# Kernel optimization log

Measured on AMD Instinct MI355X. Metric: run time of the kernel, lower is better.

Reference implementation:

```python
import jax, jax.numpy as jnp
import numpy as np

D_MODEL = 2048
NUM_HEADS = 16
HEAD_DIM = 128


def setup_inputs() -> dict:
    key = jax.random.key(0)
    ks = jax.random.split(key, 9)
    B, S = 2, 2048
    s_in = 1.0 / np.sqrt(D_MODEL)
    return {
        "x": jax.random.normal(ks[0], (B, S, D_MODEL), dtype=jnp.float32),
        "wq": jax.random.normal(ks[1], (D_MODEL, D_MODEL), dtype=jnp.float32) * s_in,
        "bq": jnp.zeros((D_MODEL,), jnp.float32),
        "wk": jax.random.normal(ks[2], (D_MODEL, HEAD_DIM), dtype=jnp.float32) * s_in,
        "bk": jnp.zeros((HEAD_DIM,), jnp.float32),
        "wv": jax.random.normal(ks[3], (D_MODEL, HEAD_DIM), dtype=jnp.float32) * s_in,
        "bv": jnpp_zeros(ks) if False else jnp.zeros((HEAD_DIM,), jnp.float32),
        "wo": jax.random.normal(ks[4], (D_MODEL, D_MODEL), dtype=jnp.float32) * s_in,
        "bo": jnp.zeros((D_MODEL,), jnp.float32),
    }


def reference(x, wq, bq, wk, bk, wv, bv, wo, bo):
    B, S, _ = x.shape
    H, Dh = NUM_HEADS, HEAD_DIM
    q = (x @ wq + bq).reshape(B, S, H, Dh)          # [B,S,H,Dh]
    k = x @ wk + bk                                  # [B,S,Dh] (single KV head)
    v = x @ wv + bv                                  # [B,S,Dh]
    scale = 1.0 / jnp.sqrt(jnp.asarray(Dh, x.dtype))
    # scores: [B,H,Sq,Sk] — MQA: K shared across heads
    scores = jnp.einsum('bqhd,bkd->bhqk', q, k) * scale
    attn = jax.nn.softmax(scores, axis=-1)
    out = jnp.einsum('bhqk,bkd->bqhd', attn, v).reshape(B, S, H * Dh)
    return out @ wo + bo
```

## Files before the change

kernel.cpp:

```cpp
#include <hip/hip_runtime.h>
#include <stdint.h>

typedef unsigned short u16;

#define D_MODEL 2048
#define HEADS 16
#define HDIM 128
#define SEQ 2048
#define BATCH 2
#define NROWS (BATCH*SEQ)
#define QKV_N (D_MODEL + 2*HDIM)

typedef __attribute__((ext_vector_type(8))) short bf16x8;
typedef __attribute__((ext_vector_type(4))) float f32x4;

__device__ inline u16 f2bf(float f) {
  union { float f; uint32_t u; } v; v.f = f;
  uint32_t r = v.u + 0x7FFFu + ((v.u >> 16) & 1u);
  return (u16)(r >> 16);
}
__device__ inline u16 f2bf_fast(float f) {
  union { float f; uint32_t u; } v; v.f = f;
  return (u16)((v.u + 0x8000u) >> 16);
}

__device__ inline void gload_lds16(const void* g, void* l) {
  __builtin_amdgcn_global_load_lds(
      (const __attribute__((address_space(1))) unsigned int*)g,
      (__attribute__((address_space(3))) unsigned int*)l, 16, 0, 0);
}

__global__ void prep_all(const float* __restrict__ x, u16* __restrict__ xb,
                         const float* __restrict__ wq, const float* __restrict__ wk,
                         const float* __restrict__ wv, const float* __restrict__ wo,
                         u16* __restrict__ wqkvT, u16* __restrict__ woT,
                         const float* __restrict__ bq, const float* __restrict__ bk,
                         const float* __restrict__ bv, float* __restrict__ biasq) {
  const int bid = blockIdx.x, tid = threadIdx.x;
  if (bid < 1024) {
    const float4* xf = (const float4*)x;
    ushort4* xo = (ushort4*)xb;
    int i = bid * 256 + tid;
#pragma unroll
    for (int r = 0; r < 8; r++, i += 262144) {
      float4 f = xf[i];
      ushort4 u;
      u.x = f2bf(f.x); u.y = f2bf(f.y); u.z = f2bf(f.z); u.w = f2bf(f.w);
      xo[i] = u;
    }
  } else if (bid < 9728) {
    __shared__ float t[32][33];
    const int b2 = bid - 1024;
    const int n0v = (b2 % 136) * 32, k0 = (b2 / 136) * 32;
    const float* src; int N, n0, drow; u16* dst;
    if (n0v < 2048)      { src = wq; N = 2048; n0 = n0v;        dst = wqkvT; drow = n0v; }
    else if (n0v < 2176) { src = wk; N = 128;  n0 = n0v - 2048; dst = wqkvT; drow = n0v; }
    else if (n0v < 2304) { src = wv; N = 128;  n0 = n0v - 2176; dst = wqkvT; drow = n0v; }
    else                 { src = wo; N = 2048; n0 = n0v - 2304; dst = woT;   drow = n0v - 2304; }
    const int tx = tid & 31, ty = tid >> 5;
#pragma unroll
    for (int i = 0; i < 4; i++)
      t[ty + 8*i][tx] = src[(size_t)(k0 + ty + 8*i) * N + n0 + tx];
    __syncthreads();
#pragma unroll
    for (int i = 0; i < 4; i++)
      dst[(size_t)(drow + ty + 8*i) * D_MODEL + k0 + tx] = f2bf(t[tx][ty + 8*i]);
  } else {
    for (int i = tid; i < QKV_N; i += 256)
      biasq[i] = (i < D_MODEL) ? bq[i]
               : ((i < D_MODEL + HDIM) ? bk[i - D_MODEL] : bv[i - D_MODEL - HDIM]);
  }
}

#define BM 128
#define BN 128
#define BKK 64

template <bool DB>
__global__ __launch_bounds__(256) void gemm_bt(
    const u16* __restrict__ A, const u16* __restrict__ BT,
    const float* __restrict__ bias,
    u16* __restrict__ Cb, float* __restrict__ Cf,
    u16* __restrict__ vT,
    int M, int N, int tilesN, int K) {
  __shared__ __align__(16) u16 sA[DB ? 2 : 1][BM * BKK];
  __shared__ __align__(16) u16 sB[DB ? 2 : 1][BN * BKK];
  const int tid = threadIdx.x;
  const int wave = tid >> 6, lane = tid & 63;
  const int bm = blockIdx.x / tilesN, bn = blockIdx.x % tilesN;
  const int m0 = bm * BM, n0 = bn * BN;
  const int wm = (wave & 1) * 64, wn = (wave >> 1) * 64;
  const int l16 = lane & 15, quad = lane >> 4;

  f32x4 acc[4][4] = {};

  const int dRow = lane >> 3;
  const int dCol = ((lane & 7) ^ (lane >> 3)) * 8;

#define GDMA(i, buf)                                                           \
  {                                                                            \
    const int _k0 = (i) * BKK;                                                 \
    _Pragma("unroll") for (int c = 0; c < 4; c++) {                            \
      const int op = wave * 4 + c;                                             \
      const int row = op * 8 + dRow;                                           \
      gload_lds16(&A[(size_t)(m0 + row) * K + _k0 + dCol], &sA[buf][op * 512]);\
      gload_lds16(&BT[(size_t)(n0 + row) * K + _k0 + dCol], &sB[buf][op * 512]);\
    }                                                                          \
  }

  const int NI = K / BKK;
  GDMA(0, 0);
  for (int i = 0; i < NI; i++) {
    const int cur = DB ? (i & 1) : 0;
    __syncthreads();
    if (DB && i + 1 < NI) GDMA(i + 1, cur ^ 1);
#pragma unroll
    for (int kk2 = 0; kk2 < 2; kk2++) {
      bf16x8 af[4], bfr[4];
#pragma unroll
      for (int mb = 0; mb < 4; ++mb) {
        const int R = wm + mb * 16 + l16;
        const int s = (kk2 * 4 + quad) ^ (l16 & 7);
        af[mb] = *(const bf16x8*)&sA[cur][R * BKK + s * 8];
      }
#pragma unroll
      for (int nb = 0; nb < 4; ++nb) {
        const int R = wn + nb * 16 + l16;
        const int s = (kk2 * 4 + quad) ^ (l16 & 7);
        bfr[nb] = *(const bf16x8*)&sB[cur][R * BKK + s * 8];
      }
#pragma unroll
      for (int mb = 0; mb < 4; ++mb)
#pragma unroll
        for (int nb = 0; nb < 4; ++nb)
          acc[mb][nb] = __builtin_amdgcn_mfma_f32_16x16x32_bf16(af[mb], bfr[nb], acc[mb][nb], 0, 0, 0);
    }
    if (!DB) {
      __syncthreads();
      if (i + 1 < NI) GDMA(i + 1, 0);
    }
  }
#undef GDMA

#pragma unroll
  for (int mb = 0; mb < 4; ++mb) {
#pragma unroll
    for (int nb = 0; nb < 4; ++nb) {
      const int gn = n0 + wn + nb * 16 + l16;
      const float bb = bias ? bias[gn] : 0.0f;
#pragma unroll
      for (int r = 0; r < 4; ++r) {
        const int gm = m0 + wm + mb * 16 + quad * 4 + r;
        const float v = acc[mb][nb][r] + bb;
        if (Cf) {
          Cf[(size_t)gm * N + gn] = v;
        } else {
          const u16 u = f2bf(v);
          Cb[(size_t)gm * N + gn] = u;
          if (vT && gn >= D_MODEL + HDIM) {
            const int bi = gm >> 11, si = gm & 2047;
            vT[((size_t)bi * HDIM + (gn - D_MODEL - HDIM)) * SEQ + si] = u;
          }
        }
      }
    }
  }
}

__global__ __launch_bounds__(256) void mqa_attn(
    const u16* __restrict__ qkv, const u16* __restrict__ vT, u16* __restrict__ ctx) {
  __shared__ __align__(16) u16 sK[2][64 * 128];
  __shared__ __align__(16) u16 sV[128 * 64];
  __shared__ __align__(16) u16 sP[4][32 * 64];
  const int tid = threadIdx.x, wave = tid >> 6, lane = tid & 63;
  const int qt = blockIdx.x & 15;
  const int h  = (blockIdx.x >> 4) & 15;
  const int b  = blockIdx.x >> 8;
  const int bS = b * SEQ;
  const int q0 = qt * 128 + wave * 32;
  const int l16 = lane & 15, quad = lane >> 4;
  const int sw = l16 & 7;
  u16* myP = &sP[wave][0];

  bf16x8 qf[2][4];
#pragma unroll
  for (int mb = 0; mb < 2; mb++)
#pragma unroll
    for (int kc = 0; kc < 4; kc++)
      qf[mb][kc] = *(const bf16x8*)&qkv[(size_t)(bS + q0 + mb*16 + l16) * QKV_N
                                        + h*HDIM + kc*32 + quad*8];

  f32x4 o[2][8] = {};
  float lrow[2] = {0.f, 0.f};
  const float sc2 = 0.08838834764831845f * 1.4426950408889634f;

  const u16* Kbase = qkv + (size_t)bS * QKV_N + D_MODEL;
  const u16* Vbase = vT + (size_t)b * HDIM * SEQ;

  const int kRowIn = lane >> 4;
  const int kChS   = lane & 15;
  const int vRowIn = lane >> 3;
  const int vChL   = (lane & 7) ^ (lane >> 3);

#define DMA_K(t, dst)                                                          \
  {                                                                            \
    const int _sk = (t) * 64;                                                  \
    _Pragma("unroll") for (int j = 0; j < 4; j++) {                            \
      const int i = wave * 4 + j;                                              \
      const int krow = i * 4 + kRowIn;                                         \
      const int kcl = kChS ^ (krow & 15);                                      \
      gload_lds16(&Kbase[(size_t)(_sk + krow) * QKV_N + kcl * 8],              \
                  &(dst)[i * 512]);                                            \
    }                                                                          \
  }
#define DMA_V(t)                                                               \
  {                                                                            \
    const int _sk = (t) * 64;                                                  \
    _Pragma("unroll") for (int j = 0; j < 4; j++) {                            \
      const int i = wave * 4 + j;                                              \
      const int d = i * 8 + vRowIn;                                            \
      gload_lds16(&Vbase[(size_t)d * SEQ + _sk + vChL * 8], &sV[i * 512]);     \
    }                                                                          \
  }

  DMA_K(0, sK[0]);
  DMA_V(0);
  __syncthreads();

  const int T = SEQ / 64;
  for (int t = 0; t < T; ++t) {
    const int cur = t & 1;
    if (t + 1 < T) DMA_K(t + 1, sK[cur ^ 1]);

    f32x4 sc[2][4];
    __builtin_amdgcn_s_setprio(1);
#pragma unroll
    for (int nb = 0; nb < 4; nb++) {
      bf16x8 kf[4];
#pragma unroll
      for (int kc = 0; kc < 4; kc++)
        kf[kc] = *(const bf16x8*)&sK[cur][(nb*16 + l16) * 128 + (((kc*4 + quad) ^ l16) * 8)];
#pragma unroll
      for (int mb = 0; mb < 2; mb++) {
        f32x4 a = {0.f, 0.f, 0.f, 0.f};
#pragma unroll
        for (int kc = 0; kc < 4; kc++)
          a = __builtin_amdgcn_mfma_f32_16x16x32_bf16(kf[kc], qf[mb][kc], a, 0, 0, 0);
        sc[mb][nb] = a;
      }
    }
    __builtin_amdgcn_s_setprio(0);

#pragma unroll
    for (int mb = 0; mb < 2; mb++)
#pragma unroll
      for (int nb = 0; nb < 4; nb++) {
        float p0 = __builtin_amdgcn_exp2f(sc[mb][nb][0] * sc2);
        float p1 = __builtin_amdgcn_exp2f(sc[mb][nb][1] * sc2);
        float p2 = __builtin_amdgcn_exp2f(sc[mb][nb][2] * sc2);
        float p3 = __builtin_amdgcn_exp2f(sc[mb][nb][3] * sc2);
        lrow[mb] += (p0 + p1) + (p2 + p3);
        uint32_t lo = (uint32_t)f2bf_fast(p0) | ((uint32_t)f2bf_fast(p1) << 16);
        uint32_t hi = (uint32_t)f2bf_fast(p2) | ((uint32_t)f2bf_fast(p3) << 16);
        uint2 w; w.x = lo; w.y = hi;
        const int pr = (nb*2 + (quad >> 1)) ^ sw;
        *(uint2*)&myP[(mb*16 + l16) * 64 + pr * 8 + (quad & 1) * 4] = w;
      }

    __syncthreads();

    bf16x8 pf[2][2];
#pragma unroll
    for (int mb = 0; mb < 2; mb++)
#pragma unroll
      for (int kc = 0; kc < 2; kc++)
        pf[mb][kc] = *(const bf16x8*)&myP[(mb*16 + l16) * 64 + (((kc*4 + quad) ^ sw) * 8)];

    __builtin_amdgcn_s_setprio(1);
#pragma unroll
    for (int nb = 0; nb < 8; nb++) {
      bf16x8 vf[2];
#pragma unroll
      for (int kc = 0; kc < 2; kc++)
        vf[kc] = *(const bf16x8*)&sV[(nb*16 + l16) * 64 + (((kc*4 + quad) ^ (l16 & 7)) * 8)];
#pragma unroll
      for (int mb = 0; mb < 2; mb++)
#pragma unroll
        for (int kc = 0; kc < 2; kc++)
          o[mb][nb] = __builtin_amdgcn_mfma_f32_16x16x32_bf16(pf[mb][kc], vf[kc], o[mb][nb], 0, 0, 0);
    }
    __builtin_amdgcn_s_setprio(0);

    __syncthreads();
    if (t + 1 < T) DMA_V(t + 1);
  }

#pragma unroll
  for (int mb = 0; mb < 2; mb++) {
    lrow[mb] += __shfl_xor(lrow[mb], 16, 64);
    lrow[mb] += __shfl_xor(lrow[mb], 32, 64);
  }
  float invl[2][4];
#pragma unroll
  for (int mb = 0; mb < 2; mb++)
#pragma unroll
    for (int r = 0; r < 4; r++)
      invl[mb][r] = 1.0f / __shfl(lrow[mb], quad * 4 + r, 64);

#pragma unroll
  for (int mb = 0; mb < 2; mb++)
#pragma unroll
    for (int nb = 0; nb < 8; nb++)
#pragma unroll
      for (int r = 0; r < 4; r++) {
        const int gq = q0 + mb*16 + quad*4 + r;
        const int gd = h * HDIM + nb*16 + l16;
        ctx[(size_t)(bS + gq) * D_MODEL + gd] = f2bf(o[mb][nb][r] * invl[mb][r]);
      }
}

extern "C" void kernel_launch(void* const* d_in, const int* in_sizes, int n_in,
                              void* d_out, int out_size, void* d_ws, size_t ws_size,
                              hipStream_t stream) {
  const float* x  = (const float*)d_in[0];
  const float* wq = (const float*)d_in[1];
  const float* bq = (const float*)d_in[2];
  const float* wk = (const float*)d_in[3];
  const float* bk = (const float*)d_in[4];
  const float* wv = (const float*)d_in[5];
  const float* bv = (const float*)d_in[6];
  const float* wo = (const float*)d_in[7];
  const float* bo = (const float*)d_in[8];
  float* out = (float*)d_out;
  char* ws = (char*)d_ws;

  u16*   xb    = (u16*)(ws + 0);
  u16*   wqkvT = (u16*)(ws + 16777216);
  u16*   woT   = (u16*)(ws + 26214400);
  u16*   qkv   = (u16*)(ws + 34603008);
  u16*   vT    = (u16*)(ws + 53477376);
  u16*   ctx   = (u16*)(ws + 54525952);
  float* biasq = (float*)(ws + 71303168);

  prep_all<<<9729, 256, 0, stream>>>(x, xb, wq, wk, wv, wo, wqkvT, woT,
                                     bq, bk, bv, biasq);
  gemm_bt<false><<<32 * 18, 256, 0, stream>>>(xb, wqkvT, biasq, qkv, nullptr, vT,
                                              NROWS, QKV_N, 18, D_MODEL);
  mqa_attn<<<BATCH * HEADS * (SEQ / 128), 256, 0, stream>>>(qkv, vT, ctx);
  gemm_bt<true><<<32 * 16, 256, 0, stream>>>(ctx, woT, bo, nullptr, out, nullptr,
                                             NROWS, D_MODEL, 16, D_MODEL);
}
```

Baseline: 302.1 us.

## Halve attention query tile, read V directly from global, raise occupancy

Result: slower. 464.0 us (+53.6%).

```diff
diff --git a/kernel.cpp b/kernel.cpp
--- a/kernel.cpp
+++ b/kernel.cpp
@@ -167,31 +167,28 @@
   }
 }
 
-__global__ __launch_bounds__(256) void mqa_attn(
+__global__ __launch_bounds__(256, 4) void mqa_attn(
     const u16* __restrict__ qkv, const u16* __restrict__ vT, u16* __restrict__ ctx) {
   __shared__ __align__(16) u16 sK[2][64 * 128];
-  __shared__ __align__(16) u16 sV[128 * 64];
-  __shared__ __align__(16) u16 sP[4][32 * 64];
+  __shared__ __align__(16) u16 sP[4][16 * 64];
   const int tid = threadIdx.x, wave = tid >> 6, lane = tid & 63;
-  const int qt = blockIdx.x & 15;
-  const int h  = (blockIdx.x >> 4) & 15;
-  const int b  = blockIdx.x >> 8;
+  const int qt = blockIdx.x & 31;
+  const int h  = (blockIdx.x >> 5) & 15;
+  const int b  = blockIdx.x >> 9;
   const int bS = b * SEQ;
-  const int q0 = qt * 128 + wave * 32;
+  const int q0 = qt * 64 + wave * 16;
   const int l16 = lane & 15, quad = lane >> 4;
   const int sw = l16 & 7;
   u16* myP = &sP[wave][0];
 
-  bf16x8 qf[2][4];
-#pragma unroll
-  for (int mb = 0; mb < 2; mb++)
-#pragma unroll
-    for (int kc = 0; kc < 4; kc++)
-      qf[mb][kc] = *(const bf16x8*)&qkv[(size_t)(bS + q0 + mb*16 + l16) * QKV_N
-                                        + h*HDIM + kc*32 + quad*8];
-
-  f32x4 o[2][8] = {};
-  float lrow[2] = {0.f, 0.f};
+  bf16x8 qf[4];
+#pragma unroll
+  for (int kc = 0; kc < 4; kc++)
+    qf[kc] = *(const bf16x8*)&qkv[(size_t)(bS + q0 + l16) * QKV_N
+                                  + h*HDIM + kc*32 + quad*8];
+
+  f32x4 o[8] = {};
+  float lrow = 0.f;
   const float sc2 = 0.08838834764831845f * 1.4426950408889634f;
 
   const u16* Kbase = qkv + (size_t)bS * QKV_N + D_MODEL;
@@ -199,8 +196,6 @@
 
   const int kRowIn = lane >> 4;
   const int kChS   = lane & 15;
-  const int vRowIn = lane >> 3;
-  const int vChL   = (lane & 7) ^ (lane >> 3);
 
 #define DMA_K(t, dst)                                                          \
   {                                                                            \
@@ -213,18 +208,8 @@
                   &(dst)[i * 512]);                                            \
     }                                                                          \
   }
-#define DMA_V(t)                                                               \
-  {                                                                            \
-    const int _sk = (t) * 64;                                                  \
-    _Pragma("unroll") for (int j = 0; j < 4; j++) {                            \
-      const int i = wave * 4 + j;                                              \
-      const int d = i * 8 + vRowIn;                                            \
-      gload_lds16(&Vbase[(size_t)d * SEQ + _sk + vChL * 8], &sV[i * 512]);     \
-    }                                                                          \
-  }
 
   DMA_K(0, sK[0]);
-  DMA_V(0);
   __syncthreads();
 
   const int T = SEQ / 64;
@@ -232,91 +217,69 @@
     const int cur = t & 1;
     if (t + 1 < T) DMA_K(t + 1, sK[cur ^ 1]);
 
-    f32x4 sc[2][4];
-    __builtin_amdgcn_s_setprio(1);
+    f32x4 sc[4];
 #pragma unroll
     for (int nb = 0; nb < 4; nb++) {
       bf16x8 kf[4];
 #pragma unroll
       for (int kc = 0; kc < 4; kc++)
         kf[kc] = *(const bf16x8*)&sK[cur][(nb*16 + l16) * 128 + (((kc*4 + quad) ^ l16) * 8)];
-#pragma unroll
-      for (int mb = 0; mb < 2; mb++) {
-        f32x4 a = {0.f, 0.f, 0.f, 0.f};
-#pragma unroll
-        for (int kc = 0; kc < 4; kc++)
-          a = __builtin_amdgcn_mfma_f32_16x16x32_bf16(kf[kc], qf[mb][kc], a, 0, 0, 0);
-        sc[mb][nb] = a;
-      }
-    }
-    __builtin_amdgcn_s_setprio(0);
-
-#pragma unroll
-    for (int mb = 0; mb < 2; mb++)
-#pragma unroll
-      for (int nb = 0; nb < 4; nb++) {
-        float p0 = __builtin_amdgcn_exp2f(sc[mb][nb][0] * sc2);
-        float p1 = __builtin_amdgcn_exp2f(sc[mb][nb][1] * sc2);
-        float p2 = __builtin_amdgcn_exp2f(sc[mb][nb][2] * sc2);
-        float p3 = __builtin_amdgcn_exp2f(sc[mb][nb][3] * sc2);
-        lrow[mb] += (p0 + p1) + (p2 + p3);
-        uint32_t lo = (uint32_t)f2bf_fast(p0) | ((uint32_t)f2bf_fast(p1) << 16);
-        uint32_t hi = (uint32_t)f2bf_fast(p2) | ((uint32_t)f2bf_fast(p3) << 16);
-        uint2 w; w.x = lo; w.y = hi;
-        const int pr = (nb*2 + (quad >> 1)) ^ sw;
-        *(uint2*)&myP[(mb*16 + l16) * 64 + pr * 8 + (quad & 1) * 4] = w;
-      }
-
-    __syncthreads();
-
-    bf16x8 pf[2][2];
-#pragma unroll
-    for (int mb = 0; mb < 2; mb++)
-#pragma unroll
-      for (int kc = 0; kc < 2; kc++)
-        pf[mb][kc] = *(const bf16x8*)&myP[(mb*16 + l16) * 64 + (((kc*4 + quad) ^ sw) * 8)];
-
-    __builtin_amdgcn_s_setprio(1);
+      f32x4 a = {0.f, 0.f, 0.f, 0.f};
+#pragma unroll
+      for (int kc = 0; kc < 4; kc++)
+        a = __builtin_amdgcn_mfma_f32_16x16x32_bf16(kf[kc], qf[kc], a, 0, 0, 0);
+      sc[nb] = a;
+    }
+
+#pragma unroll
+    for (int nb = 0; nb < 4; nb++) {
+      float p0 = __builtin_amdgcn_exp2f(sc[nb][0] * sc2);
+      float p1 = __builtin_amdgcn_exp2f(sc[nb][1] * sc2);
+      float p2 = __builtin_amdgcn_exp2f(sc[nb][2] * sc2);
+      float p3 = __builtin_amdgcn_exp2f(sc[nb][3] * sc2);
+      lrow += (p0 + p1) + (p2 + p3);
+      uint32_t lo = (uint32_t)f2bf_fast(p0) | ((uint32_t)f2bf_fast(p1) << 16);
+      uint32_t hi = (uint32_t)f2bf_fast(p2) | ((uint32_t)f2bf_fast(p3) << 16);
+      uint2 w; w.x = lo; w.y = hi;
+      const int pr = (nb*2 + (quad >> 1)) ^ sw;
+      *(uint2*)&myP[l16 * 64 + pr * 8 + (quad & 1) * 4] = w;
+    }
+
+    bf16x8 pf[2];
+#pragma unroll
+    for (int kc = 0; kc < 2; kc++)
+      pf[kc] = *(const bf16x8*)&myP[l16 * 64 + (((kc*4 + quad) ^ sw) * 8)];
+
 #pragma unroll
     for (int nb = 0; nb < 8; nb++) {
       bf16x8 vf[2];
 #pragma unroll
       for (int kc = 0; kc < 2; kc++)
-        vf[kc] = *(const bf16x8*)&sV[(nb*16 + l16) * 64 + (((kc*4 + quad) ^ (l16 & 7)) * 8)];
-#pragma unroll
-      for (int mb = 0; mb < 2; mb++)
-#pragma unroll
-        for (int kc = 0; kc < 2; kc++)
-          o[mb][nb] = __builtin_amdgcn_mfma_f32_16x16x32_bf16(pf[mb][kc], vf[kc], o[mb][nb], 0, 0, 0);
-    }
-    __builtin_amdgcn_s_setprio(0);
+        vf[kc] = *(const bf16x8*)&Vbase[(size_t)(nb*16 + l16) * SEQ
+                                        + t*64 + (kc*4 + quad) * 8];
+#pragma unroll
+      for (int kc = 0; kc < 2; kc++)
+        o[nb] = __builtin_amdgcn_mfma_f32_16x16x32_bf16(pf[kc], vf[kc], o[nb], 0, 0, 0);
+    }
 
     __syncthreads();
-    if (t + 1 < T) DMA_V(t + 1);
-  }
-
-#pragma unroll
-  for (int mb = 0; mb < 2; mb++) {
-    lrow[mb] += __shfl_xor(lrow[mb], 16, 64);
-    lrow[mb] += __shfl_xor(lrow[mb], 32, 64);
-  }
-  float invl[2][4];
-#pragma unroll
-  for (int mb = 0; mb < 2; mb++)
-#pragma unroll
-    for (int r = 0; r < 4; r++)
-      invl[mb][r] = 1.0f / __shfl(lrow[mb], quad * 4 + r, 64);
-
-#pragma unroll
-  for (int mb = 0; mb < 2; mb++)
-#pragma unroll
-    for (int nb = 0; nb < 8; nb++)
-#pragma unroll
-      for (int r = 0; r < 4; r++) {
-        const int gq = q0 + mb*16 + quad*4 + r;
-        const int gd = h * HDIM + nb*16 + l16;
-        ctx[(size_t)(bS + gq) * D_MODEL + gd] = f2bf(o[mb][nb][r] * invl[mb][r]);
-      }
+  }
+
+  lrow += __shfl_xor(lrow, 16, 64);
+  lrow += __shfl_xor(lrow, 32, 64);
+  float invl[4];
+#pragma unroll
+  for (int r = 0; r < 4; r++)
+    invl[r] = 1.0f / __shfl(lrow, quad * 4 + r, 64);
+
+#pragma unroll
+  for (int nb = 0; nb < 8; nb++)
+#pragma unroll
+    for (int r = 0; r < 4; r++) {
+      const int gq = q0 + quad*4 + r;
+      const int gd = h * HDIM + nb*16 + l16;
+      ctx[(size_t)(bS + gq) * D_MODEL + gd] = f2bf(o[nb][r] * invl[r]);
+    }
 }
 
 extern "C" void kernel_launch(void* const* d_in, const int* in_sizes, int n_in,
@@ -346,7 +309,7 @@
                                      bq, bk, bv, biasq);
   gemm_bt<false><<<32 * 18, 256, 0, stream>>>(xb, wqkvT, biasq, qkv, nullptr, vT,
                                               NROWS, QKV_N, 18, D_MODEL);
-  mqa_attn<<<BATCH * HEADS * (SEQ / 128), 256, 0, stream>>>(qkv, vT, ctx);
+  mqa_attn<<<BATCH * HEADS * (SEQ / 64), 256, 0, stream>>>(qkv, vT, ctx);
   gemm_bt<true><<<32 * 16, 256, 0, stream>>>(ctx, woT, bo, nullptr, out, nullptr,
                                              NROWS, D_MODEL, 16, D_MODEL);
 }
```

## Share K/V tiles across eight heads per block and fold softmax scale into Wq

Applied to the files above, without the earlier changes.

Result: no change. 301.6 us (-0.1%).

```diff
diff --git a/kernel.cpp b/kernel.cpp
--- a/kernel.cpp
+++ b/kernel.cpp
@@ -10,6 +10,8 @@
 #define BATCH 2
 #define NROWS (BATCH*SEQ)
 #define QKV_N (D_MODEL + 2*HDIM)
+
+#define SC2F 0.12751743f
 
 typedef __attribute__((ext_vector_type(8))) short bf16x8;
 typedef __attribute__((ext_vector_type(4))) float f32x4;
@@ -52,8 +54,8 @@
     __shared__ float t[32][33];
     const int b2 = bid - 1024;
     const int n0v = (b2 % 136) * 32, k0 = (b2 / 136) * 32;
-    const float* src; int N, n0, drow; u16* dst;
-    if (n0v < 2048)      { src = wq; N = 2048; n0 = n0v;        dst = wqkvT; drow = n0v; }
+    const float* src; int N, n0, drow; u16* dst; float scl = 1.0f;
+    if (n0v < 2048)      { src = wq; N = 2048; n0 = n0v;        dst = wqkvT; drow = n0v; scl = SC2F; }
     else if (n0v < 2176) { src = wk; N = 128;  n0 = n0v - 2048; dst = wqkvT; drow = n0v; }
     else if (n0v < 2304) { src = wv; N = 128;  n0 = n0v - 2176; dst = wqkvT; drow = n0v; }
     else                 { src = wo; N = 2048; n0 = n0v - 2304; dst = woT;   drow = n0v - 2304; }
@@ -64,10 +66,10 @@
     __syncthreads();
 #pragma unroll
     for (int i = 0; i < 4; i++)
-      dst[(size_t)(drow + ty + 8*i) * D_MODEL + k0 + tx] = f2bf(t[tx][ty + 8*i]);
+      dst[(size_t)(drow + ty + 8*i) * D_MODEL + k0 + tx] = f2bf(t[tx][ty + 8*i] * scl);
   } else {
     for (int i = tid; i < QKV_N; i += 256)
-      biasq[i] = (i < D_MODEL) ? bq[i]
+      biasq[i] = (i < D_MODEL) ? bq[i] * SC2F
                : ((i < D_MODEL + HDIM) ? bk[i - D_MODEL] : bv[i - D_MODEL - HDIM]);
   }
 }
@@ -167,17 +169,18 @@
   }
 }
 
-__global__ __launch_bounds__(256) void mqa_attn(
+__global__ __launch_bounds__(512, 2) void mqa_attn(
     const u16* __restrict__ qkv, const u16* __restrict__ vT, u16* __restrict__ ctx) {
   __shared__ __align__(16) u16 sK[2][64 * 128];
   __shared__ __align__(16) u16 sV[128 * 64];
-  __shared__ __align__(16) u16 sP[4][32 * 64];
+  __shared__ __align__(16) u16 sP[8][32 * 64];
   const int tid = threadIdx.x, wave = tid >> 6, lane = tid & 63;
-  const int qt = blockIdx.x & 15;
-  const int h  = (blockIdx.x >> 4) & 15;
-  const int b  = blockIdx.x >> 8;
+  const int qt = blockIdx.x & 63;
+  const int hg = (blockIdx.x >> 6) & 1;
+  const int b  = blockIdx.x >> 7;
   const int bS = b * SEQ;
-  const int q0 = qt * 128 + wave * 32;
+  const int h  = hg * 8 + wave;
+  const int q0 = qt * 32;
   const int l16 = lane & 15, quad = lane >> 4;
   const int sw = l16 & 7;
   u16* myP = &sP[wave][0];
@@ -192,7 +195,6 @@
 
   f32x4 o[2][8] = {};
   float lrow[2] = {0.f, 0.f};
-  const float sc2 = 0.08838834764831845f * 1.4426950408889634f;
 
   const u16* Kbase = qkv + (size_t)bS * QKV_N + D_MODEL;
   const u16* Vbase = vT + (size_t)b * HDIM * SEQ;
@@ -205,8 +207,8 @@
 #define DMA_K(t, dst)                                                          \
   {                                                                            \
     const int _sk = (t) * 64;                                                  \
-    _Pragma("unroll") for (int j = 0; j < 4; j++) {                            \
-      const int i = wave * 4 + j;                                              \
+    _Pragma("unroll") for (int j = 0; j < 2; j++) {                            \
+      const int i = wave * 2 + j;                                              \
       const int krow = i * 4 + kRowIn;                                         \
       const int kcl = kChS ^ (krow & 15);                                      \
       gload_lds16(&Kbase[(size_t)(_sk + krow) * QKV_N + kcl * 8],              \
@@ -216,8 +218,8 @@
 #define DMA_V(t)                                                               \
   {                                                                            \
     const int _sk = (t) * 64;                                                  \
-    _Pragma("unroll") for (int j = 0; j < 4; j++) {                            \
-      const int i = wave * 4 + j;                                              \
+    _Pragma("unroll") for (int j = 0; j < 2; j++) {                            \
+      const int i = wave * 2 + j;                                              \
       const int d = i * 8 + vRowIn;                                            \
       gload_lds16(&Vbase[(size_t)d * SEQ + _sk + vChL * 8], &sV[i * 512]);     \
     }                                                                          \
@@ -233,7 +235,6 @@
     if (t + 1 < T) DMA_K(t + 1, sK[cur ^ 1]);
 
     f32x4 sc[2][4];
-    __builtin_amdgcn_s_setprio(1);
 #pragma unroll
     for (int nb = 0; nb < 4; nb++) {
       bf16x8 kf[4];
@@ -249,16 +250,15 @@
         sc[mb][nb] = a;
       }
     }
-    __builtin_amdgcn_s_setprio(0);
 
 #pragma unroll
     for (int mb = 0; mb < 2; mb++)
 #pragma unroll
       for (int nb = 0; nb < 4; nb++) {
-        float p0 = __builtin_amdgcn_exp2f(sc[mb][nb][0] * sc2);
-        float p1 = __builtin_amdgcn_exp2f(sc[mb][nb][1] * sc2);
-        float p2 = __builtin_amdgcn_exp2f(sc[mb][nb][2] * sc2);
-        float p3 = __builtin_amdgcn_exp2f(sc[mb][nb][3] * sc2);
+        float p0 = __builtin_amdgcn_exp2f(sc[mb][nb][0]);
+        float p1 = __builtin_amdgcn_exp2f(sc[mb][nb][1]);
+        float p2 = __builtin_amdgcn_exp2f(sc[mb][nb][2]);
+        float p3 = __builtin_amdgcn_exp2f(sc[mb][nb][3]);
         lrow[mb] += (p0 + p1) + (p2 + p3);
         uint32_t lo = (uint32_t)f2bf_fast(p0) | ((uint32_t)f2bf_fast(p1) << 16);
         uint32_t hi = (uint32_t)f2bf_fast(p2) | ((uint32_t)f2bf_fast(p3) << 16);
@@ -276,7 +276,6 @@
       for (int kc = 0; kc < 2; kc++)
         pf[mb][kc] = *(const bf16x8*)&myP[(mb*16 + l16) * 64 + (((kc*4 + quad) ^ sw) * 8)];
 
-    __builtin_amdgcn_s_setprio(1);
 #pragma unroll
     for (int nb = 0; nb < 8; nb++) {
       bf16x8 vf[2];
@@ -289,7 +288,6 @@
         for (int kc = 0; kc < 2; kc++)
           o[mb][nb] = __builtin_amdgcn_mfma_f32_16x16x32_bf16(pf[mb][kc], vf[kc], o[mb][nb], 0, 0, 0);
     }
-    __builtin_amdgcn_s_setprio(0);
 
     __syncthreads();
     if (t + 1 < T) DMA_V(t + 1);
@@ -346,7 +344,7 @@
                                      bq, bk, bv, biasq);
   gemm_bt<false><<<32 * 18, 256, 0, stream>>>(xb, wqkvT, biasq, qkv, nullptr, vT,
                                               NROWS, QKV_N, 18, D_MODEL);
-  mqa_attn<<<BATCH * HEADS * (SEQ / 128), 256, 0, stream>>>(qkv, vT, ctx);
+  mqa_attn<<<BATCH * 2 * (SEQ / 32), 512, 0, stream>>>(qkv, vT, ctx);
   gemm_bt<true><<<32 * 16, 256, 0, stream>>>(ctx, woT, bo, nullptr, out, nullptr,
                                              NROWS, D_MODEL, 16, D_MODEL);
 }
```

## Use 256x256 GEMM tiles with 512 threads and fold softmax scale into Wq

Applied to the files above, without the earlier changes.

Result: slower. 348.8 us (+15.5%).

```diff
diff --git a/kernel.cpp b/kernel.cpp
--- a/kernel.cpp
+++ b/kernel.cpp
@@ -10,6 +10,8 @@
 #define BATCH 2
 #define NROWS (BATCH*SEQ)
 #define QKV_N (D_MODEL + 2*HDIM)
+
+#define SC2F 0.12751743f
 
 typedef __attribute__((ext_vector_type(8))) short bf16x8;
 typedef __attribute__((ext_vector_type(4))) float f32x4;
@@ -52,8 +54,8 @@
     __shared__ float t[32][33];
     const int b2 = bid - 1024;
     const int n0v = (b2 % 136) * 32, k0 = (b2 / 136) * 32;
-    const float* src; int N, n0, drow; u16* dst;
-    if (n0v < 2048)      { src = wq; N = 2048; n0 = n0v;        dst = wqkvT; drow = n0v; }
+    const float* src; int N, n0, drow; u16* dst; float scl = 1.0f;
+    if (n0v < 2048)      { src = wq; N = 2048; n0 = n0v;        dst = wqkvT; drow = n0v; scl = SC2F; }
     else if (n0v < 2176) { src = wk; N = 128;  n0 = n0v - 2048; dst = wqkvT; drow = n0v; }
     else if (n0v < 2304) { src = wv; N = 128;  n0 = n0v - 2176; dst = wqkvT; drow = n0v; }
     else                 { src = wo; N = 2048; n0 = n0v - 2304; dst = woT;   drow = n0v - 2304; }
@@ -64,40 +66,39 @@
     __syncthreads();
 #pragma unroll
     for (int i = 0; i < 4; i++)
-      dst[(size_t)(drow + ty + 8*i) * D_MODEL + k0 + tx] = f2bf(t[tx][ty + 8*i]);
+      dst[(size_t)(drow + ty + 8*i) * D_MODEL + k0 + tx] = f2bf(t[tx][ty + 8*i] * scl);
   } else {
     for (int i = tid; i < QKV_N; i += 256)
-      biasq[i] = (i < D_MODEL) ? bq[i]
+      biasq[i] = (i < D_MODEL) ? bq[i] * SC2F
                : ((i < D_MODEL + HDIM) ? bk[i - D_MODEL] : bv[i - D_MODEL - HDIM]);
   }
 }
 
-#define BM 128
-#define BN 128
+#define BM2 256
+#define BN2 256
 #define BKK 64
 
-template <bool DB>
-__global__ __launch_bounds__(256) void gemm_bt(
+__global__ __launch_bounds__(512, 2) void gemm256(
     const u16* __restrict__ A, const u16* __restrict__ BT,
     const float* __restrict__ bias,
     u16* __restrict__ Cb, float* __restrict__ Cf,
     u16* __restrict__ vT,
     int M, int N, int tilesN, int K) {
-  __shared__ __align__(16) u16 sA[DB ? 2 : 1][BM * BKK];
-  __shared__ __align__(16) u16 sB[DB ? 2 : 1][BN * BKK];
+  __shared__ __align__(16) u16 sA[2][BM2 * BKK];
+  __shared__ __align__(16) u16 sB[2][BN2 * BKK];
   const int tid = threadIdx.x;
   const int wave = tid >> 6, lane = tid & 63;
   const int bm = blockIdx.x / tilesN, bn = blockIdx.x % tilesN;
-  const int m0 = bm * BM, n0 = bn * BN;
-  const int wm = (wave & 1) * 64, wn = (wave >> 1) * 64;
+  const int m0 = bm * BM2, n0 = bn * BN2;
+  const int wm = (wave >> 2) * 128, wn = (wave & 3) * 64;
   const int l16 = lane & 15, quad = lane >> 4;
 
-  f32x4 acc[4][4] = {};
+  f32x4 acc[8][4] = {};
 
   const int dRow = lane >> 3;
   const int dCol = ((lane & 7) ^ (lane >> 3)) * 8;
 
-#define GDMA(i, buf)                                                           \
+#define GDMA2(i, buf)                                                          \
   {                                                                            \
     const int _k0 = (i) * BKK;                                                 \
     _Pragma("unroll") for (int c = 0; c < 4; c++) {                            \
@@ -109,20 +110,14 @@
   }
 
   const int NI = K / BKK;
-  GDMA(0, 0);
+  GDMA2(0, 0);
   for (int i = 0; i < NI; i++) {
-    const int cur = DB ? (i & 1) : 0;
+    const int cur = i & 1;
     __syncthreads();
-    if (DB && i + 1 < NI) GDMA(i + 1, cur ^ 1);
+    if (i + 1 < NI) GDMA2(i + 1, cur ^ 1);
 #pragma unroll
     for (int kk2 = 0; kk2 < 2; kk2++) {
-      bf16x8 af[4], bfr[4];
-#pragma unroll
-      for (int mb = 0; mb < 4; ++mb) {
-        const int R = wm + mb * 16 + l16;
-        const int s = (kk2 * 4 + quad) ^ (l16 & 7);
-        af[mb] = *(const bf16x8*)&sA[cur][R * BKK + s * 8];
-      }
+      bf16x8 bfr[4];
 #pragma unroll
       for (int nb = 0; nb < 4; ++nb) {
         const int R = wn + nb * 16 + l16;
@@ -130,20 +125,20 @@
         bfr[nb] = *(const bf16x8*)&sB[cur][R * BKK + s * 8];
       }
 #pragma unroll
-      for (int mb = 0; mb < 4; ++mb)
+      for (int mb = 0; mb < 8; ++mb) {
+        const int R = wm + mb * 16 + l16;
+        const int s = (kk2 * 4 + quad) ^ (l16 & 7);
+        bf16x8 af = *(const bf16x8*)&sA[cur][R * BKK + s * 8];
 #pragma unroll
         for (int nb = 0; nb < 4; ++nb)
-          acc[mb][nb] = __builtin_amdgcn_mfma_f32_16x16x32_bf16(af[mb], bfr[nb], acc[mb][nb], 0, 0, 0);
-    }
-    if (!DB) {
-      __syncthreads();
-      if (i + 1 < NI) GDMA(i + 1, 0);
-    }
-  }
-#undef GDMA
-
-#pragma unroll
-  for (int mb = 0; mb < 4; ++mb) {
+          acc[mb][nb] = __builtin_amdgcn_mfma_f32_16x16x32_bf16(af, bfr[nb], acc[mb][nb], 0, 0, 0);
+      }
+    }
+  }
+#undef GDMA2
+
+#pragma unroll
+  for (int mb = 0; mb < 8; ++mb) {
 #pragma unroll
     for (int nb = 0; nb < 4; ++nb) {
       const int gn = n0 + wn + nb * 16 + l16;
@@ -192,7 +187,6 @@
 
   f32x4 o[2][8] = {};
   float lrow[2] = {0.f, 0.f};
-  const float sc2 = 0.08838834764831845f * 1.4426950408889634f;
 
   const u16* Kbase = qkv + (size_t)bS * QKV_N + D_MODEL;
   const u16* Vbase = vT + (size_t)b * HDIM * SEQ;
@@ -233,7 +227,6 @@
     if (t + 1 < T) DMA_K(t + 1, sK[cur ^ 1]);
 
     f32x4 sc[2][4];
-    __builtin_amdgcn_s_setprio(1);
 #pragma unroll
     for (int nb = 0; nb < 4; nb++) {
       bf16x8 kf[4];
@@ -249,16 +242,15 @@
         sc[mb][nb] = a;
       }
     }
-    __builtin_amdgcn_s_setprio(0);
 
 #pragma unroll
     for (int mb = 0; mb < 2; mb++)
 #pragma unroll
       for (int nb = 0; nb < 4; nb++) {
-        float p0 = __builtin_amdgcn_exp2f(sc[mb][nb][0] * sc2);
-        float p1 = __builtin_amdgcn_exp2f(sc[mb][nb][1] * sc2);
-        float p2 = __builtin_amdgcn_exp2f(sc[mb][nb][2] * sc2);
-        float p3 = __builtin_amdgcn_exp2f(sc[mb][nb][3] * sc2);
+        float p0 = __builtin_amdgcn_exp2f(sc[mb][nb][0]);
+        float p1 = __builtin_amdgcn_exp2f(sc[mb][nb][1]);
+        float p2 = __builtin_amdgcn_exp2f(sc[mb][nb][2]);
+        float p3 = __builtin_amdgcn_exp2f(sc[mb][nb][3]);
         lrow[mb] += (p0 + p1) + (p2 + p3);
         uint32_t lo = (uint32_t)f2bf_fast(p0) | ((uint32_t)f2bf_fast(p1) << 16);
         uint32_t hi = (uint32_t)f2bf_fast(p2) | ((uint32_t)f2bf_fast(p3) << 16);
@@ -276,7 +268,6 @@
       for (int kc = 0; kc < 2; kc++)
         pf[mb][kc] = *(const bf16x8*)&myP[(mb*16 + l16) * 64 + (((kc*4 + quad) ^ sw) * 8)];
 
-    __builtin_amdgcn_s_setprio(1);
 #pragma unroll
     for (int nb = 0; nb < 8; nb++) {
       bf16x8 vf[2];
@@ -289,7 +280,6 @@
         for (int kc = 0; kc < 2; kc++)
           o[mb][nb] = __builtin_amdgcn_mfma_f32_16x16x32_bf16(pf[mb][kc], vf[kc], o[mb][nb], 0, 0, 0);
     }
-    __builtin_amdgcn_s_setprio(0);
 
     __syncthreads();
     if (t + 1 < T) DMA_V(t + 1);
@@ -344,9 +334,9 @@
 
   prep_all<<<9729, 256, 0, stream>>>(x, xb, wq, wk, wv, wo, wqkvT, woT,
                                      bq, bk, bv, biasq);
-  gemm_bt<false><<<32 * 18, 256, 0, stream>>>(xb, wqkvT, biasq, qkv, nullptr, vT,
-                                              NROWS, QKV_N, 18, D_MODEL);
+  gemm256<<<16 * 9, 512, 0, stream>>>(xb, wqkvT, biasq, qkv, nullptr, vT,
+                                      NROWS, QKV_N, 9, D_MODEL);
   mqa_attn<<<BATCH * HEADS * (SEQ / 128), 256, 0, stream>>>(qkv, vT, ctx);
-  gemm_bt<true><<<32 * 16, 256, 0, stream>>>(ctx, woT, bo, nullptr, out, nullptr,
-                                             NROWS, D_MODEL, 16, D_MODEL);
-}
+  gemm256<<<16 * 8, 512, 0, stream>>>(ctx, woT, bo, nullptr, out, nullptr,
+                                      NROWS, D_MODEL, 8, D_MODEL);
+}
```
